# Kernel optimization log

Measured on AMD Instinct MI355X. Metric: run time of the kernel, lower is better.

## Reference

```python
import jax, jax.numpy as jnp
import numpy as np

N = 50000      # nodes
E = 800000     # edges (avg degree 16)
D_IN, D_H, D_OUT = 128, 128, 64


def setup_inputs() -> dict:
    key = jax.random.key(0)
    ks = jax.random.split(key, 12)
    s = 0.05  # weight init scale
    return {
        "x": jax.random.normal(ks[0], (N, D_IN), jnp.float32),
        "edge_index": jax.random.randint(ks[1], (2, E), 0, N, dtype=jnp.int64),
        "Wl0": jax.random.normal(ks[2], (D_H, D_IN), jnp.float32) * s,
        "bl0": jax.random.normal(ks[3], (D_H,), jnp.float32) * s,
        "Wr0": jax.random.normal(ks[4], (D_H, D_IN), jnp.float32) * s,
        "Wl1": jax.random.normal(ks[5], (D_H, D_H), jnp.float32) * s,
        "bl1": jax.random.normal(ks[6], (D_H,), jnp.float32) * s,
        "Wr1": jax.random.normal(ks[7], (D_H, D_H), jnp.float32) * s,
        "Wl2": jax.random.normal(ks[8], (D_OUT, D_H), jnp.float32) * s,
        "bl2": jax.random.normal(ks[9], (D_OUT,), jnp.float32) * s,
        "Wr2": jax.random.normal(ks[10], (D_OUT, D_H), jnp.float32) * s,
    }


def _sage_layer(h, src, dst, Wl, bl, Wr):
    # mean aggregation over incoming neighbors: out[i] = mean_{j in N(i)} h[j]
    n = h.shape[0]
    agg = jax.ops.segment_sum(h[src], dst, num_segments=n)          # [N, D]
    deg = jax.ops.segment_sum(jnp.ones((src.shape[0],), h.dtype), dst,
                              num_segments=n)                        # [N]
    mean = agg / jnp.maximum(deg, 1.0)[:, None]  # empty rows -> 0, matches torch_sparse
    # lin_l(agg) + lin_r(self); lin_r has no bias in PyG SAGEConv
    return mean @ Wl.T + bl + h @ Wr.T


def reference(x, edge_index, Wl0, bl0, Wr0, Wl1, bl1, Wr1, Wl2, bl2, Wr2):
    src, dst = edge_index[1], edge_index[0]  # adj row = dst, col = src
    h = jax.nn.relu(_sage_layer(x, src, dst, Wl0, bl0, Wr0))
    h = jax.nn.relu(_sage_layer(h, src, dst, Wl1, bl1, Wr1))
    h = _sage_layer(h, src, dst, Wl2, bl2, Wr2)
    return jax.nn.log_softmax(h, axis=1)
```

## Files before the change

### kernel.cpp

```cpp
#include <hip/hip_runtime.h>
#include <hip/hip_bf16.h>


typedef __attribute__((ext_vector_type(8))) short bf16x8;
typedef __attribute__((ext_vector_type(4))) float f32x4;

#define NPB 128
#define BCAP 2560
#define EPB 8192
#define EPT 32
#define CPAD 16

__device__ __forceinline__ unsigned short f2bf(float f) {
    unsigned int u = __builtin_bit_cast(unsigned int, f);
    u += 0x7fffu + ((u >> 16) & 1u);
    return (unsigned short)(u >> 16);
}
__device__ __forceinline__ float bf2f(unsigned int bits16) {
    return __builtin_bit_cast(float, bits16 << 16);
}
__device__ __forceinline__ bf16x8 pack8(float4 lo, float4 hi) {
    bf16x8 r;
    r[0] = (short)f2bf(lo.x); r[1] = (short)f2bf(lo.y);
    r[2] = (short)f2bf(lo.z); r[3] = (short)f2bf(lo.w);
    r[4] = (short)f2bf(hi.x); r[5] = (short)f2bf(hi.y);
    r[6] = (short)f2bf(hi.z); r[7] = (short)f2bf(hi.w);
    return r;
}


__global__ __launch_bounds__(256) void distribute_kernel(const int* __restrict__ dst,
                                                         const int* __restrict__ srcv,
                                                         int* __restrict__ gcnt,
                                                         unsigned int* __restrict__ staging,
                                                         int E, int NBc) {
    __shared__ unsigned int stage[EPB];
    __shared__ int hist[400];
    __shared__ int lstart[400];
    __shared__ int gbase[400];
    __shared__ int scanbuf[256];
    int t = threadIdx.x;
    int e0 = blockIdx.x * EPB;
    unsigned int w[EPT];

    for (int b = t; b < NBc + 1; b += 256) hist[b] = 0;
    __syncthreads();

#pragma unroll
    for (int i = 0; i < EPT; ++i) {
        int e = e0 + i * 256 + t;
        unsigned int word = 0xFFFFFFFFu;
        if (e < E) word = ((unsigned int)dst[e] << 16) | (unsigned int)srcv[e];
        w[i] = word;
        int b = (int)(word >> 23); if (b > NBc) b = NBc;
        atomicAdd(&hist[b], 1);
    }
    __syncthreads();

    int b0 = 2 * t, b1 = 2 * t + 1;
    int h0 = (b0 <= NBc) ? hist[b0] : 0;
    int h1 = (b1 <= NBc) ? hist[b1] : 0;
    int pair = h0 + h1;
    scanbuf[t] = pair;
    __syncthreads();
    for (int off = 1; off < 256; off <<= 1) {
        int v = (t >= off) ? scanbuf[t - off] : 0;
        __syncthreads();
        scanbuf[t] += v;
        __syncthreads();
    }
    int excl = scanbuf[t] - pair;
    if (b0 <= NBc) lstart[b0] = excl;
    if (b1 <= NBc) lstart[b1] = excl + h0;
    __syncthreads();

    for (int b = t; b < NBc; b += 256) {
        int h = hist[b];
        gbase[b] = h ? atomicAdd(&gcnt[b * CPAD], h) : 0;
    }
    for (int b = t; b < NBc + 1; b += 256) hist[b] = lstart[b];
    __syncthreads();

#pragma unroll
    for (int i = 0; i < EPT; ++i) {
        unsigned int word = w[i];
        int b = (int)(word >> 23); if (b > NBc) b = NBc;
        int p = atomicAdd(&hist[b], 1);
        stage[p] = word;
    }
    __syncthreads();

    int total = lstart[NBc];
    for (int i = t; i < total; i += 256) {
        unsigned int word = stage[i];
        int b = (int)(word >> 23);
        int gpos = gbase[b] + (i - lstart[b]);
        staging[(size_t)b * BCAP + gpos] = word;
    }
}


__global__ __launch_bounds__(256) void build_kernel(const unsigned int* __restrict__ staging,
                                                    const int* __restrict__ gcnt,
                                                    int* __restrict__ row_ptr,
                                                    int* __restrict__ adj, int N, int NBc) {
    __shared__ int hist[NPB];
    __shared__ int scn[NPB];
    __shared__ int wsum[4];
    int b = blockIdx.x;
    int t = threadIdx.x;
    int n0 = b * NPB;
    int nb = N - n0; if (nb > NPB) nb = NPB;
    int ec = gcnt[b * CPAD];
    const unsigned int* st = staging + (size_t)b * BCAP;

    int a = 0;
    for (int j = t; j < b; j += 256) a += gcnt[j * CPAD];
#pragma unroll
    for (int off = 32; off; off >>= 1) a += __shfl_xor(a, off);
    if ((t & 63) == 0) wsum[t >> 6] = a;
    if (t < NPB) hist[t] = 0;
    __syncthreads();
    int bb = wsum[0] + wsum[1] + wsum[2] + wsum[3];

    for (int i = t; i < ec; i += 256)
        atomicAdd(&hist[(st[i] >> 16) & (NPB - 1)], 1);
    __syncthreads();

    int v = (t < NPB) ? hist[t] : 0;
    if (t < NPB) scn[t] = v;
    __syncthreads();
    for (int off = 1; off < NPB; off <<= 1) {
        int u = (t >= off && t < NPB) ? scn[t - off] : 0;
        __syncthreads();
        if (t < NPB) scn[t] += u;
        __syncthreads();
    }
    if (t < NPB) hist[t] = scn[t] - v;
    if (t < nb) row_ptr[n0 + t] = bb + (scn[t] - v);
    if (b == NBc - 1 && t == 0) row_ptr[N] = bb + ec;
    __syncthreads();

    for (int i = t; i < ec; i += 256) {
        unsigned int pk = st[i];
        int p = atomicAdd(&hist[(pk >> 16) & (NPB - 1)], 1);
        adj[bb + p] = (int)(pk & 0xffffu);
    }
}


__global__ void cast_w_kernel(const float* p0, const float* p1, const float* p2,
                              const float* p3, const float* p4, const float* p5,
                              unsigned short* __restrict__ wbf) {
    int w = blockIdx.x * 256 + threadIdx.x;
    if (w < 40960) {
        const float* src;
        int local;
        if      (w < 8192)  { src = p0; local = w; }
        else if (w < 16384) { src = p1; local = w - 8192; }
        else if (w < 24576) { src = p2; local = w - 16384; }
        else if (w < 32768) { src = p3; local = w - 24576; }
        else if (w < 36864) { src = p4; local = w - 32768; }
        else                { src = p5; local = w - 36864; }
        float2 v = ((const float2*)src)[local];
        unsigned int p = (unsigned int)f2bf(v.x) | ((unsigned int)f2bf(v.y) << 16);
        ((unsigned int*)wbf)[w] = p;
    }
}


template<int CF, int AF32>
__global__ __launch_bounds__(256) void gemm_mfma_kernel(const void* __restrict__ Hp,
                                                        const unsigned short* __restrict__ Wl,
                                                        const unsigned short* __restrict__ Wr,
                                                        unsigned short* __restrict__ C,
                                                        int N) {
    int wave = threadIdx.x >> 6;
    int lane = threadIdx.x & 63;
    int l15 = lane & 15, quad = lane >> 4;
    const int NCOL = 4 * CF * 16;
    const int half = NCOL >> 1;
    int m0 = blockIdx.x * 64;

    bf16x8 bfr[CF][4];
#pragma unroll
    for (int cf = 0; cf < CF; ++cf) {
        int col0 = (wave * CF + cf) * 16;
        const unsigned short* W = (col0 < half) ? Wl : Wr;
        int wr = (col0 < half ? col0 : col0 - half) + l15;
#pragma unroll
        for (int ks = 0; ks < 4; ++ks)
            bfr[cf][ks] = ((const bf16x8*)(W + (size_t)wr * 128))[ks * 4 + quad];
    }

    f32x4 acc[4][CF] = {};

    if constexpr (AF32) {
#pragma unroll
        for (int h = 0; h < 2; ++h) {
            float4 fa[2][4][2];
#pragma unroll
            for (int p = 0; p < 2; ++p) {
                int rf = h * 2 + p;
                int r0 = m0 + rf * 16 + l15; if (r0 > N - 1) r0 = N - 1;
                const float4* A = (const float4*)((const float*)Hp + (size_t)r0 * 128);
#pragma unroll
                for (int ks = 0; ks < 4; ++ks) {
                    int vidx = ks * 4 + quad;
                    fa[p][ks][0] = A[vidx * 2];
                    fa[p][ks][1] = A[vidx * 2 + 1];
                }
            }
#pragma unroll
            for (int p = 0; p < 2; ++p) {
                int rf = h * 2 + p;
#pragma unroll
                for (int ks = 0; ks < 4; ++ks) {
                    bf16x8 a = pack8(fa[p][ks][0], fa[p][ks][1]);
#pragma unroll
                    for (int cf = 0; cf < CF; ++cf)
                        acc[rf][cf] = __builtin_amdgcn_mfma_f32_16x16x32_bf16(a, bfr[cf][ks],
                                                                              acc[rf][cf], 0, 0, 0);
                }
            }
        }
    } else {
        bf16x8 afr[4][4];
#pragma unroll
        for (int rf = 0; rf < 4; ++rf) {
            int r0 = m0 + rf * 16 + l15; if (r0 > N - 1) r0 = N - 1;
            const bf16x8* A = (const bf16x8*)((const unsigned short*)Hp + (size_t)r0 * 128);
#pragma unroll
            for (int ks = 0; ks < 4; ++ks)
                afr[rf][ks] = A[ks * 4 + quad];
        }
#pragma unroll
        for (int rf = 0; rf < 4; ++rf)
#pragma unroll
            for (int ks = 0; ks < 4; ++ks)
#pragma unroll
                for (int cf = 0; cf < CF; ++cf)
                    acc[rf][cf] = __builtin_amdgcn_mfma_f32_16x16x32_bf16(afr[rf][ks], bfr[cf][ks],
                                                                          acc[rf][cf], 0, 0, 0);
    }

#pragma unroll
    for (int rf = 0; rf < 4; ++rf)
#pragma unroll
        for (int cf = 0; cf < CF; ++cf)
#pragma unroll
            for (int r = 0; r < 4; ++r) {
                int row = m0 + rf * 16 + quad * 4 + r;
                if (row < N)
                    C[(size_t)row * NCOL + (wave * CF + cf) * 16 + l15] = f2bf(acc[rf][cf][r]);
            }
}


__global__ __launch_bounds__(256) void agg_relu_kernel(const unsigned short* __restrict__ C,
                                                       const int* __restrict__ row_ptr,
                                                       const int* __restrict__ adj,
                                                       const float* __restrict__ bias,
                                                       unsigned short* __restrict__ hout, int N) {
    int node = (int)((blockIdx.x * blockDim.x + threadIdx.x) >> 6);
    int lane = threadIdx.x & 63;
    if (node >= N) return;
    int g = lane >> 4;
    int c = lane & 15;
    int beg = row_ptr[node], end = row_ptr[node + 1];
    float p[8] = {};

    int e = beg;
    while (e < end) {
        int cnt = end - e; if (cnt > 64) cnt = 64;
        int ll = lane; if (ll > cnt - 1) ll = cnt - 1;
        int myidx = adj[e + ll];
        int c1 = cnt - 1;
        for (int i = 0; i < cnt; i += 16) {
            int t0 = i + g, t1 = i + 4 + g, t2 = i + 8 + g, t3 = i + 12 + g;
            int s0 = __shfl(myidx, t0 > c1 ? c1 : t0);
            int s1 = __shfl(myidx, t1 > c1 ? c1 : t1);
            int s2 = __shfl(myidx, t2 > c1 ? c1 : t2);
            int s3 = __shfl(myidx, t3 > c1 ? c1 : t3);
            float m0 = t0 < cnt ? 1.f : 0.f;
            float m1 = t1 < cnt ? 1.f : 0.f;
            float m2 = t2 < cnt ? 1.f : 0.f;
            float m3 = t3 < cnt ? 1.f : 0.f;
            bf16x8 v0 = ((const bf16x8*)(C + (size_t)s0 * 256))[c];
            bf16x8 v1 = ((const bf16x8*)(C + (size_t)s1 * 256))[c];
            bf16x8 v2 = ((const bf16x8*)(C + (size_t)s2 * 256))[c];
            bf16x8 v3 = ((const bf16x8*)(C + (size_t)s3 * 256))[c];
#pragma unroll
            for (int k = 0; k < 8; ++k) {
                p[k] += m0 * bf2f((unsigned short)v0[k]);
                p[k] += m1 * bf2f((unsigned short)v1[k]);
                p[k] += m2 * bf2f((unsigned short)v2[k]);
                p[k] += m3 * bf2f((unsigned short)v3[k]);
            }
        }
        e += cnt;
    }

#pragma unroll
    for (int k = 0; k < 8; ++k) {
        p[k] += __shfl_xor(p[k], 16);
        p[k] += __shfl_xor(p[k], 32);
    }

    int deg = end - beg;
    float inv = 1.0f / (float)(deg > 1 ? deg : 1);
    bf16x8 sv = ((const bf16x8*)(C + (size_t)node * 256))[16 + c];
    float4 b0 = ((const float4*)bias)[2 * c];
    float4 b1 = ((const float4*)bias)[2 * c + 1];
    float bb[8] = {b0.x, b0.y, b0.z, b0.w, b1.x, b1.y, b1.z, b1.w};
    bf16x8 o;
#pragma unroll
    for (int k = 0; k < 8; ++k) {
        float v = fmaxf(p[k] * inv + bb[k] + bf2f((unsigned short)sv[k]), 0.f);
        o[k] = (short)f2bf(v);
    }
    if (g == 0)
        ((bf16x8*)(hout + (size_t)node * 128))[c] = o;
}


__global__ __launch_bounds__(256) void final_kernel(const unsigned short* __restrict__ C,
                                                    const int* __restrict__ row_ptr,
                                                    const int* __restrict__ adj,
                                                    const float* __restrict__ bias,
                                                    float* __restrict__ out, int N) {
    int node = (int)((blockIdx.x * blockDim.x + threadIdx.x) >> 6);
    int lane = threadIdx.x & 63;
    if (node >= N) return;
    int g = lane >> 3;
    int c = lane & 7;
    int beg = row_ptr[node], end = row_ptr[node + 1];
    float p[8] = {};

    int e = beg;
    while (e < end) {
        int cnt = end - e; if (cnt > 64) cnt = 64;
        int ll = lane; if (ll > cnt - 1) ll = cnt - 1;
        int myidx = adj[e + ll];
        int c1 = cnt - 1;
        for (int i = 0; i < cnt; i += 16) {
            int ta = i + g, tb = i + 8 + g;
            int sa = __shfl(myidx, ta > c1 ? c1 : ta);
            int sb = __shfl(myidx, tb > c1 ? c1 : tb);
            float ma = ta < cnt ? 1.f : 0.f;
            float mb = tb < cnt ? 1.f : 0.f;
            bf16x8 va = ((const bf16x8*)(C + (size_t)sa * 128))[c];
            bf16x8 vb = ((const bf16x8*)(C + (size_t)sb * 128))[c];
#pragma unroll
            for (int k = 0; k < 8; ++k) {
                p[k] += ma * bf2f((unsigned short)va[k]);
                p[k] += mb * bf2f((unsigned short)vb[k]);
            }
        }
        e += cnt;
    }

#pragma unroll
    for (int k = 0; k < 8; ++k) {
        p[k] += __shfl_xor(p[k], 8);
        p[k] += __shfl_xor(p[k], 16);
        p[k] += __shfl_xor(p[k], 32);
    }

    int deg = end - beg;
    float inv = 1.0f / (float)(deg > 1 ? deg : 1);
    bf16x8 sv = ((const bf16x8*)(C + (size_t)node * 128))[8 + c];
    float4 b0 = ((const float4*)bias)[2 * c];
    float4 b1 = ((const float4*)bias)[2 * c + 1];
    float bb[8] = {b0.x, b0.y, b0.z, b0.w, b1.x, b1.y, b1.z, b1.w};
    float u[8];
#pragma unroll
    for (int k = 0; k < 8; ++k)
        u[k] = p[k] * inv + bb[k] + bf2f((unsigned short)sv[k]);

    float m = u[0];
#pragma unroll
    for (int k = 1; k < 8; ++k) m = fmaxf(m, u[k]);
#pragma unroll
    for (int off = 1; off < 8; off <<= 1) m = fmaxf(m, __shfl_xor(m, off));
    float se = 0.f;
#pragma unroll
    for (int k = 0; k < 8; ++k) se += __expf(u[k] - m);
#pragma unroll
    for (int off = 1; off < 8; off <<= 1) se += __shfl_xor(se, off);
    float ls = __logf(se);

    if (g == 0) {
        float4 o0 = {u[0] - m - ls, u[1] - m - ls, u[2] - m - ls, u[3] - m - ls};
        float4 o1 = {u[4] - m - ls, u[5] - m - ls, u[6] - m - ls, u[7] - m - ls};
        ((float4*)(out + (size_t)node * 64))[2 * c] = o0;
        ((float4*)(out + (size_t)node * 64))[2 * c + 1] = o1;
    }
}


extern "C" void kernel_launch(void* const* d_in, const int* in_sizes, int n_in,
                              void* d_out, int out_size, void* d_ws, size_t ws_size,
                              hipStream_t stream) {
    const float* x   = (const float*)d_in[0];
    const int*   ei  = (const int*)d_in[1];
    const float* Wl0 = (const float*)d_in[2];
    const float* bl0 = (const float*)d_in[3];
    const float* Wr0 = (const float*)d_in[4];
    const float* Wl1 = (const float*)d_in[5];
    const float* bl1 = (const float*)d_in[6];
    const float* Wr1 = (const float*)d_in[7];
    const float* Wl2 = (const float*)d_in[8];
    const float* bl2 = (const float*)d_in[9];
    const float* Wr2 = (const float*)d_in[10];
    float* out = (float*)d_out;

    const int N  = in_sizes[0] / 128;
    const int E  = in_sizes[1] / 2;
    const int NB = (N + NPB - 1) / NPB;

    char* ws = (char*)d_ws;
    auto alloc = [&](size_t bytes) {
        char* p = ws;
        ws += (bytes + 255) & ~(size_t)255;
        return p;
    };
    int*   row_ptr    = (int*)alloc((size_t)(N + 1) * 4);
    int*   adj        = (int*)alloc((size_t)E * 4);
    int*   gcnt       = (int*)alloc((size_t)NB * CPAD * 4);
    unsigned int* staging = (unsigned int*)alloc((size_t)NB * BCAP * 4);
    unsigned short* wbf = (unsigned short*)alloc((size_t)81920 * 2);
    unsigned short* C   = (unsigned short*)alloc((size_t)N * 256 * 2);
    unsigned short* hA  = (unsigned short*)alloc((size_t)N * 128 * 2);
    unsigned short* hB  = (unsigned short*)alloc((size_t)N * 128 * 2);

    const int* dstp = ei;
    const int* srcp = ei + E;

    hipMemsetAsync(gcnt, 0, (size_t)NB * CPAD * 4, stream);
    int distBlocks = (E + EPB - 1) / EPB;
    distribute_kernel<<<distBlocks, 256, 0, stream>>>(dstp, srcp, gcnt, staging, E, NB);
    build_kernel<<<NB, 256, 0, stream>>>(staging, gcnt, row_ptr, adj, N, NB);

    cast_w_kernel<<<160, 256, 0, stream>>>(Wl0, Wr0, Wl1, Wr1, Wl2, Wr2, wbf);
    unsigned short* wl0 = wbf;
    unsigned short* wr0 = wbf + 16384;
    unsigned short* wl1 = wbf + 32768;
    unsigned short* wr1 = wbf + 49152;
    unsigned short* wl2 = wbf + 65536;
    unsigned short* wr2 = wbf + 73728;

    dim3 blk(256);
    int gemmRows = (N + 63) / 64;
    int aggBlocks = (N * 64 + 255) / 256;

    gemm_mfma_kernel<4, 1><<<gemmRows, blk, 0, stream>>>((const void*)x, wl0, wr0, C, N);
    agg_relu_kernel<<<aggBlocks, blk, 0, stream>>>(C, row_ptr, adj, bl0, hA, N);
    gemm_mfma_kernel<4, 0><<<gemmRows, blk, 0, stream>>>((const void*)hA, wl1, wr1, C, N);
    agg_relu_kernel<<<aggBlocks, blk, 0, stream>>>(C, row_ptr, adj, bl1, hB, N);
    gemm_mfma_kernel<2, 0><<<gemmRows, blk, 0, stream>>>((const void*)hB, wl2, wr2, C, N);
    final_kernel<<<aggBlocks, blk, 0, stream>>>(C, row_ptr, adj, bl2, out, N);
}
```

Baseline: 276.2 us.

## Merge weight cast into distribute and CSR build into first GEMM launch

Folds the weight bf16 cast into the edge-distribute kernel as extra blocks, and runs the CSR build blocks together with the first-layer GEMM blocks in one launch, since neither pair depends on the other. This removes two kernel launches and lets the independent small build work overlap with the GEMM. It also adds a min-blocks hint of 2 to the GEMM launch bounds, which may limit register allocation for the GEMM body.

```diff
diff --git a/kernel.cpp b/kernel.cpp
--- a/kernel.cpp
+++ b/kernel.cpp
@@ -29,18 +29,42 @@
 }
 
 
-__global__ __launch_bounds__(256) void distribute_kernel(const int* __restrict__ dst,
-                                                         const int* __restrict__ srcv,
-                                                         int* __restrict__ gcnt,
-                                                         unsigned int* __restrict__ staging,
-                                                         int E, int NBc) {
+__global__ __launch_bounds__(256) void dist_cast_kernel(const int* __restrict__ dst,
+                                                        const int* __restrict__ srcv,
+                                                        int* __restrict__ gcnt,
+                                                        unsigned int* __restrict__ staging,
+                                                        int E, int NBc, int DB,
+                                                        const float* p0, const float* p1,
+                                                        const float* p2, const float* p3,
+                                                        const float* p4, const float* p5,
+                                                        unsigned short* __restrict__ wbf) {
     __shared__ unsigned int stage[EPB];
     __shared__ int hist[400];
     __shared__ int lstart[400];
     __shared__ int gbase[400];
     __shared__ int scanbuf[256];
+    int bid = blockIdx.x;
     int t = threadIdx.x;
-    int e0 = blockIdx.x * EPB;
+
+    if (bid >= DB) {
+        int w = (bid - DB) * 256 + t;
+        if (w < 40960) {
+            const float* src;
+            int local;
+            if      (w < 8192)  { src = p0; local = w; }
+            else if (w < 16384) { src = p1; local = w - 8192; }
+            else if (w < 24576) { src = p2; local = w - 16384; }
+            else if (w < 32768) { src = p3; local = w - 24576; }
+            else if (w < 36864) { src = p4; local = w - 32768; }
+            else                { src = p5; local = w - 36864; }
+            float2 v = ((const float2*)src)[local];
+            unsigned int p = (unsigned int)f2bf(v.x) | ((unsigned int)f2bf(v.y) << 16);
+            ((unsigned int*)wbf)[w] = p;
+        }
+        return;
+    }
+
+    int e0 = bid * EPB;
     unsigned int w[EPT];
 
     for (int b = t; b < NBc + 1; b += 256) hist[b] = 0;
@@ -100,87 +124,18 @@
 }
 
 
-__global__ __launch_bounds__(256) void build_kernel(const unsigned int* __restrict__ staging,
-                                                    const int* __restrict__ gcnt,
-                                                    int* __restrict__ row_ptr,
-                                                    int* __restrict__ adj, int N, int NBc) {
-    __shared__ int hist[NPB];
-    __shared__ int scn[NPB];
-    __shared__ int wsum[4];
-    int b = blockIdx.x;
-    int t = threadIdx.x;
-    int n0 = b * NPB;
-    int nb = N - n0; if (nb > NPB) nb = NPB;
-    int ec = gcnt[b * CPAD];
-    const unsigned int* st = staging + (size_t)b * BCAP;
-
-    int a = 0;
-    for (int j = t; j < b; j += 256) a += gcnt[j * CPAD];
-#pragma unroll
-    for (int off = 32; off; off >>= 1) a += __shfl_xor(a, off);
-    if ((t & 63) == 0) wsum[t >> 6] = a;
-    if (t < NPB) hist[t] = 0;
-    __syncthreads();
-    int bb = wsum[0] + wsum[1] + wsum[2] + wsum[3];
-
-    for (int i = t; i < ec; i += 256)
-        atomicAdd(&hist[(st[i] >> 16) & (NPB - 1)], 1);
-    __syncthreads();
-
-    int v = (t < NPB) ? hist[t] : 0;
-    if (t < NPB) scn[t] = v;
-    __syncthreads();
-    for (int off = 1; off < NPB; off <<= 1) {
-        int u = (t >= off && t < NPB) ? scn[t - off] : 0;
-        __syncthreads();
-        if (t < NPB) scn[t] += u;
-        __syncthreads();
-    }
-    if (t < NPB) hist[t] = scn[t] - v;
-    if (t < nb) row_ptr[n0 + t] = bb + (scn[t] - v);
-    if (b == NBc - 1 && t == 0) row_ptr[N] = bb + ec;
-    __syncthreads();
-
-    for (int i = t; i < ec; i += 256) {
-        unsigned int pk = st[i];
-        int p = atomicAdd(&hist[(pk >> 16) & (NPB - 1)], 1);
-        adj[bb + p] = (int)(pk & 0xffffu);
-    }
-}
-
-
-__global__ void cast_w_kernel(const float* p0, const float* p1, const float* p2,
-                              const float* p3, const float* p4, const float* p5,
-                              unsigned short* __restrict__ wbf) {
-    int w = blockIdx.x * 256 + threadIdx.x;
-    if (w < 40960) {
-        const float* src;
-        int local;
-        if      (w < 8192)  { src = p0; local = w; }
-        else if (w < 16384) { src = p1; local = w - 8192; }
-        else if (w < 24576) { src = p2; local = w - 16384; }
-        else if (w < 32768) { src = p3; local = w - 24576; }
-        else if (w < 36864) { src = p4; local = w - 32768; }
-        else                { src = p5; local = w - 36864; }
-        float2 v = ((const float2*)src)[local];
-        unsigned int p = (unsigned int)f2bf(v.x) | ((unsigned int)f2bf(v.y) << 16);
-        ((unsigned int*)wbf)[w] = p;
-    }
-}
-
-
 template<int CF, int AF32>
-__global__ __launch_bounds__(256) void gemm_mfma_kernel(const void* __restrict__ Hp,
-                                                        const unsigned short* __restrict__ Wl,
-                                                        const unsigned short* __restrict__ Wr,
-                                                        unsigned short* __restrict__ C,
-                                                        int N) {
+__device__ __forceinline__ void gemm_body(int mb,
+                                          const void* __restrict__ Hp,
+                                          const unsigned short* __restrict__ Wl,
+                                          const unsigned short* __restrict__ Wr,
+                                          unsigned short* __restrict__ C, int N) {
     int wave = threadIdx.x >> 6;
     int lane = threadIdx.x & 63;
     int l15 = lane & 15, quad = lane >> 4;
     const int NCOL = 4 * CF * 16;
     const int half = NCOL >> 1;
-    int m0 = blockIdx.x * 64;
+    int m0 = mb * 64;
 
     bf16x8 bfr[CF][4];
 #pragma unroll
@@ -254,6 +209,77 @@
                 if (row < N)
                     C[(size_t)row * NCOL + (wave * CF + cf) * 16 + l15] = f2bf(acc[rf][cf][r]);
             }
+}
+
+
+template<int CF, int AF32>
+__global__ __launch_bounds__(256, 2) void build_gemm_kernel(const unsigned int* __restrict__ staging,
+                                                            const int* __restrict__ gcnt,
+                                                            int* __restrict__ row_ptr,
+                                                            int* __restrict__ adj, int N, int NBc,
+                                                            const void* __restrict__ Hp,
+                                                            const unsigned short* __restrict__ Wl,
+                                                            const unsigned short* __restrict__ Wr,
+                                                            unsigned short* __restrict__ C) {
+    __shared__ int hist[NPB];
+    __shared__ int scn[NPB];
+    __shared__ int wsum[4];
+    int bid = blockIdx.x;
+    int t = threadIdx.x;
+
+    if (bid >= NBc) {
+        gemm_body<CF, AF32>(bid - NBc, Hp, Wl, Wr, C, N);
+        return;
+    }
+
+    int b = bid;
+    int n0 = b * NPB;
+    int nb = N - n0; if (nb > NPB) nb = NPB;
+    int ec = gcnt[b * CPAD];
+    const unsigned int* st = staging + (size_t)b * BCAP;
+
+    int a = 0;
+    for (int j = t; j < b; j += 256) a += gcnt[j * CPAD];
+#pragma unroll
+    for (int off = 32; off; off >>= 1) a += __shfl_xor(a, off);
+    if ((t & 63) == 0) wsum[t >> 6] = a;
+    if (t < NPB) hist[t] = 0;
+    __syncthreads();
+    int bb = wsum[0] + wsum[1] + wsum[2] + wsum[3];
+
+    for (int i = t; i < ec; i += 256)
+        atomicAdd(&hist[(st[i] >> 16) & (NPB - 1)], 1);
+    __syncthreads();
+
+    int v = (t < NPB) ? hist[t] : 0;
+    if (t < NPB) scn[t] = v;
+    __syncthreads();
+    for (int off = 1; off < NPB; off <<= 1) {
+        int u = (t >= off && t < NPB) ? scn[t - off] : 0;
+        __syncthreads();
+        if (t < NPB) scn[t] += u;
+        __syncthreads();
+    }
+    if (t < NPB) hist[t] = scn[t] - v;
+    if (t < nb) row_ptr[n0 + t] = bb + (scn[t] - v);
+    if (b == NBc - 1 && t == 0) row_ptr[N] = bb + ec;
+    __syncthreads();
+
+    for (int i = t; i < ec; i += 256) {
+        unsigned int pk = st[i];
+        int p = atomicAdd(&hist[(pk >> 16) & (NPB - 1)], 1);
+        adj[bb + p] = (int)(pk & 0xffffu);
+    }
+}
+
+
+template<int CF, int AF32>
+__global__ __launch_bounds__(256, 2) void gemm_mfma_kernel(const void* __restrict__ Hp,
+                                                           const unsigned short* __restrict__ Wl,
+                                                           const unsigned short* __restrict__ Wr,
+                                                           unsigned short* __restrict__ C,
+                                                           int N) {
+    gemm_body<CF, AF32>(blockIdx.x, Hp, Wl, Wr, C, N);
 }
 
 
@@ -437,12 +463,6 @@
     const int* dstp = ei;
     const int* srcp = ei + E;
 
-    hipMemsetAsync(gcnt, 0, (size_t)NB * CPAD * 4, stream);
-    int distBlocks = (E + EPB - 1) / EPB;
-    distribute_kernel<<<distBlocks, 256, 0, stream>>>(dstp, srcp, gcnt, staging, E, NB);
-    build_kernel<<<NB, 256, 0, stream>>>(staging, gcnt, row_ptr, adj, N, NB);
-
-    cast_w_kernel<<<160, 256, 0, stream>>>(Wl0, Wr0, Wl1, Wr1, Wl2, Wr2, wbf);
     unsigned short* wl0 = wbf;
     unsigned short* wr0 = wbf + 16384;
     unsigned short* wl1 = wbf + 32768;
@@ -451,10 +471,15 @@
     unsigned short* wr2 = wbf + 73728;
 
     dim3 blk(256);
+    int DB = (E + EPB - 1) / EPB;
     int gemmRows = (N + 63) / 64;
     int aggBlocks = (N * 64 + 255) / 256;
 
-    gemm_mfma_kernel<4, 1><<<gemmRows, blk, 0, stream>>>((const void*)x, wl0, wr0, C, N);
+    hipMemsetAsync(gcnt, 0, (size_t)NB * CPAD * 4, stream);
+    dist_cast_kernel<<<DB + 160, blk, 0, stream>>>(dstp, srcp, gcnt, staging, E, NB, DB,
+                                                   Wl0, Wr0, Wl1, Wr1, Wl2, Wr2, wbf);
+    build_gemm_kernel<4, 1><<<NB + gemmRows, blk, 0, stream>>>(staging, gcnt, row_ptr, adj,
+                                                               N, NB, (const void*)x, wl0, wr0, C);
     agg_relu_kernel<<<aggBlocks, blk, 0, stream>>>(C, row_ptr, adj, bl0, hA, N);
     gemm_mfma_kernel<4, 0><<<gemmRows, blk, 0, stream>>>((const void*)hA, wl1, wr1, C, N);
     agg_relu_kernel<<<aggBlocks, blk, 0, stream>>>(C, row_ptr, adj, bl1, hB, N);
```

Measured after the change: 270.0 us. -2.2%, faster.
